# Kernel tuning notes

Hardware: AMD Instinct MI355X
Metric: run time of the kernel (lower is better)

Reference implementation:

```python
import jax, jax.numpy as jnp
import numpy as np

LN_EPS = 1e-5


def layer_norm(x, g, b):
    m = jnp.mean(x, axis=-1, keepdims=True)
    v = jnp.mean((x - m) ** 2, axis=-1, keepdims=True)
    return (x - m) * jax.lax.rsqrt(v + LN_EPS) * g + b


def setup_inputs() -> dict:
    key = jax.random.key(0)
    ks = jax.random.split(key, 8)
    B, S, D, C = 32, 512, 768, 25
    return {
        "bert_feature": jax.random.normal(ks[0], (B, S, D), dtype=jnp.float32),
        "output_encoder": jax.random.normal(ks[1], (B, S, D), dtype=jnp.float32),
        "cos_sim": jax.random.normal(ks[2], (B, S, C), dtype=jnp.float32),
        "decoder_embedding": jax.random.normal(ks[3], (B, C, D), dtype=jnp.float32),
        "labels": jax.random.randint(ks[4], (B, S), 0, C, dtype=jnp.int32),
        "ln_gamma": jnp.ones((D,), dtype=jnp.float32),
        "ln_beta": jnp.zeros((D,), dtype=jnp.float32),
        "W_add": jax.random.normal(ks[5], (D, C), dtype=jnp.float32) * 0.02,
        "b_add": jnp.zeros((C,), dtype=jnp.float32),
        "start_trans": jax.random.normal(ks[6], (C,), dtype=jnp.float32) * 0.1,
        "end_trans": jax.random.normal(ks[7], (C,), dtype=jnp.float32) * 0.1,
        "trans": jax.random.normal(jax.random.fold_in(key, 99), (C, C), dtype=jnp.float32) * 0.1,
    }


def crf_neg_log_likelihood(emissions, tags, start, end, trans):
    # emissions [B,S,C] (log-probs), tags [B,S]; no mask (all valid), torchcrf semantics
    B, S, C = emissions.shape
    b = jnp.arange(B)
    # numerator (gold path score)
    em_sc = jnp.take_along_axis(emissions, tags[:, :, None], axis=2)[..., 0].sum(axis=1)
    tr_sc = trans[tags[:, :-1], tags[:, 1:]].sum(axis=1)
    num = start[tags[:, 0]] + em_sc + tr_sc + end[tags[:, -1]]
    # partition function via forward algorithm (scan over time)
    def step(score, em_t):  # score [B,C]
        ns = jax.nn.logsumexp(score[:, :, None] + trans[None] + em_t[:, None, :], axis=1)
        return ns, None
    score0 = start[None] + emissions[:, 0]
    scoreT, _ = jax.lax.scan(step, score0, jnp.swapaxes(emissions[:, 1:], 0, 1))
    logZ = jax.nn.logsumexp(scoreT + end[None], axis=1)
    llh = num - logZ
    return llh.mean()  # reduction='mean'


def crf_decode(emissions, start, end, trans):
    # Viterbi; emissions [B,S,C]
    B, S, C = emissions.shape
    def vstep(score, em_t):
        cand = score[:, :, None] + trans[None]      # [B, prev, cur]
        best = jnp.max(cand, axis=1) + em_t
        idx = jnp.argmax(cand, axis=1)              # [B, cur] -> best prev tag
        return best, idx
    score0 = start[None] + emissions[:, 0]
    scoreT, hist = jax.lax.scan(vstep, score0, jnp.swapaxes(emissions[:, 1:], 0, 1))
    last = jnp.argmax(scoreT + end[None], axis=1)   # [B]
    def back(tag, h):
        prev = jnp.take_along_axis(h, tag[:, None], axis=1)[:, 0]
        return prev, prev
    _, prevs = jax.lax.scan(back, last, hist, reverse=True)
    return jnp.concatenate([prevs, last[None]], axis=0).T  # [B,S]


def reference(bert_feature, output_encoder, cos_sim, decoder_embedding, labels,
              ln_gamma, ln_beta, W_add, b_add, start_trans, end_trans, trans):
    # dropout is identity at eval time
    bf = layer_norm(bert_feature, ln_gamma, ln_beta)
    # prob_times_query: triple python loop == bmm(cos_sim, LN(decoder_embedding))
    # NOTE: original (faithfully) passes raw cos_sim, not its softmax.
    dec = layer_norm(decoder_embedding, ln_gamma, ln_beta)
    prob_query = jnp.einsum('bsc,bcd->bsd', cos_sim, dec)
    emb = layer_norm(bf + output_encoder + prob_query, ln_gamma, ln_beta)
    emb = jax.nn.relu(emb)
    ner_prob = jax.nn.log_softmax(emb @ W_add + b_add, axis=-1)  # [B,S,C]
    cos_sim_prob = jax.nn.softmax(cos_sim, axis=-1)
    llh = crf_neg_log_likelihood(ner_prob, labels, start_trans, end_trans, trans)
    loss = -llh  # model returns -1 * crf_loss
    path = crf_decode(cos_sim_prob, start_trans, end_trans, trans)
    return loss, path
```

## Files before the change

kernel.cpp:

```cpp
#include <hip/hip_runtime.h>
#include <hip/hip_bf16.h>


#define NEGINF (-1e30f)

__device__ __forceinline__ float rlane(float x, int i) {
  return __int_as_float(__builtin_amdgcn_readlane(__float_as_int(x), i));
}
__device__ __forceinline__ float rfl(float x) {
  return __int_as_float(__builtin_amdgcn_readfirstlane(__float_as_int(x)));
}
template <int CTRL, int RMASK>
__device__ __forceinline__ float dppAdd(float x) {
  return x + __int_as_float(__builtin_amdgcn_update_dpp(
                 0, __float_as_int(x), CTRL, RMASK, 0xF, true));
}
__device__ __forceinline__ float wsum(float v) {
  v = dppAdd<0x111, 0xF>(v);
  v = dppAdd<0x112, 0xF>(v);
  v = dppAdd<0x114, 0xF>(v);
  v = dppAdd<0x118, 0xF>(v);
  v = dppAdd<0x142, 0xA>(v);
  v = dppAdd<0x143, 0xC>(v);
  return rlane(v, 63);
}
__device__ __forceinline__ ushort f2bf(float x) {
  __hip_bfloat16 h = __float2bfloat16(x);
  return *reinterpret_cast<ushort*>(&h);
}
__device__ __forceinline__ void ld12(float* x, const float* p, int lane) {
#pragma unroll
  for (int k = 0; k < 3; k++) {
    float4 v = *(const float4*)(p + (lane + (k << 6)) * 4);
    x[4 * k + 0] = v.x; x[4 * k + 1] = v.y; x[4 * k + 2] = v.z; x[4 * k + 3] = v.w;
  }
}
__device__ __forceinline__ void ld12bf(float* x, const ushort* row, int lane) {
  uint2 d0 = *(const uint2*)((const char*)row + lane * 8);
  uint2 d1 = *(const uint2*)((const char*)row + lane * 8 + 512);
  uint2 d2 = *(const uint2*)((const char*)row + lane * 8 + 1024);
  x[0]  = __uint_as_float(d0.x << 16); x[1]  = __uint_as_float(d0.x & 0xffff0000u);
  x[2]  = __uint_as_float(d0.y << 16); x[3]  = __uint_as_float(d0.y & 0xffff0000u);
  x[4]  = __uint_as_float(d1.x << 16); x[5]  = __uint_as_float(d1.x & 0xffff0000u);
  x[6]  = __uint_as_float(d1.y << 16); x[7]  = __uint_as_float(d1.y & 0xffff0000u);
  x[8]  = __uint_as_float(d2.x << 16); x[9]  = __uint_as_float(d2.x & 0xffff0000u);
  x[10] = __uint_as_float(d2.y << 16); x[11] = __uint_as_float(d2.y & 0xffff0000u);
}

__device__ __forceinline__ float max25(const float c[25]) {
  float m0 = fmaxf(fmaxf(c[0], c[1]), c[2]);
  float m1 = fmaxf(fmaxf(c[3], c[4]), c[5]);
  float m2 = fmaxf(fmaxf(c[6], c[7]), c[8]);
  float m3 = fmaxf(fmaxf(c[9], c[10]), c[11]);
  float m4 = fmaxf(fmaxf(c[12], c[13]), c[14]);
  float m5 = fmaxf(fmaxf(c[15], c[16]), c[17]);
  float m6 = fmaxf(fmaxf(c[18], c[19]), c[20]);
  float m7 = fmaxf(fmaxf(c[21], c[22]), c[23]);
  float n0 = fmaxf(fmaxf(m0, m1), m2);
  float n1 = fmaxf(fmaxf(m3, m4), m5);
  float n2 = fmaxf(fmaxf(m6, m7), c[24]);
  return fmaxf(fmaxf(n0, n1), n2);
}

__device__ __forceinline__ void argmax25(const float c[25], float& bv, int& bi) {
  float v[13]; int x[13];
#pragma unroll
  for (int i = 0; i < 12; i++) {
    bool t = c[2 * i + 1] > c[2 * i];
    v[i] = t ? c[2 * i + 1] : c[2 * i];
    x[i] = t ? 2 * i + 1 : 2 * i;
  }
  v[12] = c[24]; x[12] = 24;
  float w[7]; int y[7];
#pragma unroll
  for (int i = 0; i < 6; i++) {
    bool t = v[2 * i + 1] > v[2 * i];
    w[i] = t ? v[2 * i + 1] : v[2 * i];
    y[i] = t ? x[2 * i + 1] : x[2 * i];
  }
  w[6] = v[12]; y[6] = x[12];
  float u[4]; int z[4];
#pragma unroll
  for (int i = 0; i < 3; i++) {
    bool t = w[2 * i + 1] > w[2 * i];
    u[i] = t ? w[2 * i + 1] : w[2 * i];
    z[i] = t ? y[2 * i + 1] : y[2 * i];
  }
  u[3] = w[6]; z[3] = y[6];
  bool t0 = u[1] > u[0]; float a = t0 ? u[1] : u[0]; int ai = t0 ? z[1] : z[0];
  bool t1 = u[3] > u[2]; float b = t1 ? u[3] : u[2]; int bj = t1 ? z[3] : z[2];
  bool t2 = b > a; bv = t2 ? b : a; bi = t2 ? bj : ai;
}

__global__ __launch_bounds__(256) void prep_kernel(
    const float* __restrict__ decemb, const float* __restrict__ gamma,
    const float* __restrict__ beta, const float* __restrict__ Wadd,
    const float* __restrict__ cosim,
    ushort* __restrict__ decb, ushort* __restrict__ wtb, float* __restrict__ csp) {
  const int blk = blockIdx.x;
  const int tid = threadIdx.x;
  __shared__ float sa[4], sq[4];
  __shared__ float sem[12800];
  if (blk < 800) {
    const float* in = decemb + (size_t)blk * 768;
    float x0 = in[tid], x1 = in[tid + 256], x2 = in[tid + 512];
    float s = x0 + x1 + x2, q = x0 * x0 + x1 * x1 + x2 * x2;
    float ws_ = wsum(s), wq = wsum(q);
    int w = tid >> 6, ln = tid & 63;
    if (ln == 0) { sa[w] = ws_; sq[w] = wq; }
    __syncthreads();
    float s1 = sa[0] + sa[1] + sa[2] + sa[3];
    float s2 = sq[0] + sq[1] + sq[2] + sq[3];
    float mean = s1 * (1.f / 768.f);
    float rstd = rsqrtf(s2 * (1.f / 768.f) - mean * mean + 1e-5f);
    ushort* o = decb + (size_t)blk * 768;
    o[tid]       = f2bf((x0 - mean) * rstd * gamma[tid]       + beta[tid]);
    o[tid + 256] = f2bf((x1 - mean) * rstd * gamma[tid + 256] + beta[tid + 256]);
    o[tid + 512] = f2bf((x2 - mean) * rstd * gamma[tid + 512] + beta[tid + 512]);
  } else if (blk < 832) {
    int gid = (blk - 800) * 256 + tid;
    for (int e = gid; e < 19200; e += 32 * 256) {
      int d = e / 25, j = e - d * 25;
      wtb[j * 768 + d] = f2bf(Wadd[e]);
    }
  } else {
    const int b = blk - 832;
    const float4* cb4 = (const float4*)(cosim + (size_t)b * 12800);
    float4* em4 = (float4*)sem;
    for (int i = tid; i < 3200; i += 256) em4[i] = cb4[i];
    __syncthreads();
#pragma unroll
    for (int rr = 0; rr < 2; rr++) {
      const int r = tid + (rr << 8);
      float v[25];
#pragma unroll
      for (int k = 0; k < 25; k++) v[k] = sem[r * 25 + k];
      float m01 = v[0];
#pragma unroll
      for (int k = 1; k < 25; k++) m01 = fmaxf(m01, v[k]);
      float s = 0.f;
#pragma unroll
      for (int k = 0; k < 25; k++) { v[k] = __expf(v[k] - m01); s += v[k]; }
      float rinv = __builtin_amdgcn_rcpf(s);
#pragma unroll
      for (int k = 0; k < 25; k++) sem[r * 25 + k] = v[k] * rinv;
    }
    __syncthreads();
    float4* cp4 = (float4*)(csp + (size_t)b * 12800);
    for (int i = tid; i < 3200; i += 256) cp4[i] = em4[i];
  }
}

__global__ __launch_bounds__(256) void main_kernel(
    const float* __restrict__ bert, const float* __restrict__ oenc,
    const float* __restrict__ cosim, const float* __restrict__ gamma,
    const float* __restrict__ beta, const float* __restrict__ badd,
    const ushort* __restrict__ decb, const ushort* __restrict__ wtb,
    const float* __restrict__ csp, const float* __restrict__ startt,
    const float* __restrict__ endt, const float* __restrict__ trans,
    float* __restrict__ nprob, float* __restrict__ traceF,
    float* __restrict__ traceB, float* __restrict__ out) {
  __shared__ ushort sh[19200];
  const int tid = threadIdx.x;
  const int lane = tid & 63;
  const int wid = tid >> 6;
  const int bid = blockIdx.x;

  if (bid < 64) {
    const bool isFwd = bid < 32;
    const int b = isFwd ? bid : bid - 32;
    const int tl = (lane < 25) ? lane : 24;
    float* em = (float*)sh;
    {
      const float4* src4 = (const float4*)(csp + (size_t)b * 12800 + (isFwd ? 0 : 6300));
      float4* dst4 = (float4*)em;
#pragma unroll
      for (int i = 0; i < 7; i++) {
        int e = tid + (i << 8);
        if (e < 1625) dst4[e] = src4[e];
      }
    }
    __syncthreads();
    if (wid != 0) return;

    __builtin_amdgcn_s_setprio(1);
    if (isFwd) {
      float* tf = traceF + (size_t)b * 16448;
      float Tc[25];
#pragma unroll
      for (int i = 0; i < 25; i++) Tc[i] = trans[i * 25 + tl];
      float sc = startt[tl] + em[tl];
      tf[lane] = sc;
      float emA = em[25 + tl], emB = em[50 + tl];
      for (int t = 1; t <= 256; t++) {
        float emC = em[(t + 2) * 25 + tl];
        float s[25], c[25];
#pragma unroll
        for (int i = 0; i < 25; i++) s[i] = rlane(sc, i);
#pragma unroll
        for (int i = 0; i < 25; i++) c[i] = s[i] + Tc[i];
        float bv = max25(c);
        sc = bv + emA;
        tf[t * 64 + lane] = sc;
        emA = emB; emB = emC;
      }
    } else {
      float* tb = traceB + (size_t)b * 16448;
      float Tr[25];
#pragma unroll
      for (int j = 0; j < 25; j++) Tr[j] = trans[tl * 25 + j];
      float bwd = endt[tl];
      float emA = em[(511 - 252) * 25 + tl], emB = em[(510 - 252) * 25 + tl];
      for (int t = 511; t >= 257; t--) {
        float emC = em[(t - 2 - 252) * 25 + tl];
        tb[(511 - t) * 64 + lane] = bwd;
        float u = bwd + emA;
        float s[25], c[25];
#pragma unroll
        for (int j = 0; j < 25; j++) s[j] = rlane(u, j);
#pragma unroll
        for (int j = 0; j < 25; j++) c[j] = s[j] + Tr[j];
        float bv = max25(c);
        bwd = bv;
        emA = emB; emB = emC;
      }
      tb[255 * 64 + lane] = bwd;
    }
    __builtin_amdgcn_s_setprio(0);
    return;
  }

  if (bid == 64 && tid == 0) out[0] = 0.f;
  const int idx = bid - 64;
  const int swz = (idx & 7) * 256 + (idx >> 3);
  const int b = swz >> 6;
  const int rowg = b * 512 + ((swz & 63) << 3) + (wid << 1);

  {
    const uint4* src = (const uint4*)(decb + (size_t)b * 19200);
    uint4* dst = (uint4*)sh;
#pragma unroll
    for (int i = 0; i < 10; i++) {
      int e = tid + (i << 8);
      if (e < 2400) dst[e] = src[e];
    }
  }
  float g[12], bbv[12];
  ld12(g, gamma, lane);
  ld12(bbv, beta, lane);
  float acc[2][12];
  ld12(acc[0], bert + (size_t)(rowg + 0) * 768, lane);
  ld12(acc[1], bert + (size_t)(rowg + 1) * 768, lane);
  float cs0 = (lane < 25) ? cosim[(size_t)(rowg + 0) * 25 + lane] : 0.f;
  float cs1 = (lane < 25) ? cosim[(size_t)(rowg + 1) * 25 + lane] : 0.f;
  __syncthreads();

#pragma unroll
  for (int r = 0; r < 2; r++) {
    float s = 0.f, q = 0.f;
#pragma unroll
    for (int e = 0; e < 12; e++) { s += acc[r][e]; q += acc[r][e] * acc[r][e]; }
    s = wsum(s); q = wsum(q);
    float mean = s * (1.f / 768.f);
    float rstd = rsqrtf(q * (1.f / 768.f) - mean * mean + 1e-5f);
#pragma unroll
    for (int e = 0; e < 12; e++) acc[r][e] = (acc[r][e] - mean) * rstd * g[e] + bbv[e];
  }

  const char* sd = (const char*)sh;
#pragma unroll 5
  for (int c = 0; c < 25; c++) {
    uint2 d0 = *(const uint2*)(sd + c * 1536 + lane * 8);
    uint2 d1 = *(const uint2*)(sd + c * 1536 + lane * 8 + 512);
    uint2 d2 = *(const uint2*)(sd + c * 1536 + lane * 8 + 1024);
    float dv[12];
    dv[0]  = __uint_as_float(d0.x << 16); dv[1]  = __uint_as_float(d0.x & 0xffff0000u);
    dv[2]  = __uint_as_float(d0.y << 16); dv[3]  = __uint_as_float(d0.y & 0xffff0000u);
    dv[4]  = __uint_as_float(d1.x << 16); dv[5]  = __uint_as_float(d1.x & 0xffff0000u);
    dv[6]  = __uint_as_float(d1.y << 16); dv[7]  = __uint_as_float(d1.y & 0xffff0000u);
    dv[8]  = __uint_as_float(d2.x << 16); dv[9]  = __uint_as_float(d2.x & 0xffff0000u);
    dv[10] = __uint_as_float(d2.y << 16); dv[11] = __uint_as_float(d2.y & 0xffff0000u);
    float f0 = rlane(cs0, c), f1 = rlane(cs1, c);
#pragma unroll
    for (int e = 0; e < 12; e++) {
      acc[0][e] = fmaf(f0, dv[e], acc[0][e]);
      acc[1][e] = fmaf(f1, dv[e], acc[1][e]);
    }
  }

#pragma unroll
  for (int r = 0; r < 2; r++) {
    float y[12];
    ld12(y, oenc + (size_t)(rowg + r) * 768, lane);
#pragma unroll
    for (int e = 0; e < 12; e++) acc[r][e] += y[e];
  }

#pragma unroll
  for (int r = 0; r < 2; r++) {
    float s = 0.f, q = 0.f;
#pragma unroll
    for (int e = 0; e < 12; e++) { s += acc[r][e]; q += acc[r][e] * acc[r][e]; }
    s = wsum(s); q = wsum(q);
    float mean = s * (1.f / 768.f);
    float rstd = rsqrtf(q * (1.f / 768.f) - mean * mean + 1e-5f);
#pragma unroll
    for (int e = 0; e < 12; e++)
      acc[r][e] = fmaxf((acc[r][e] - mean) * rstd * g[e] + bbv[e], 0.f);
  }

  __syncthreads();

  ushort* scw0 = sh + wid * 3400;
  ushort* scw1 = scw0 + 1700;
#pragma unroll 5
  for (int j = 0; j < 25; j++) {
    float wv[12];
    ld12bf(wv, wtb + j * 768, lane);
    float p0 = 0.f, p1 = 0.f;
#pragma unroll
    for (int e = 0; e < 12; e++) {
      p0 = fmaf(acc[0][e], wv[e], p0);
      p1 = fmaf(acc[1][e], wv[e], p1);
    }
    scw0[j * 68 + lane] = f2bf(p0);
    scw1[j * 68 + lane] = f2bf(p1);
  }
  float bav = (lane < 25) ? badd[lane] : 0.f;
  const int jj = (lane < 25) ? lane : 24;
#pragma unroll
  for (int r = 0; r < 2; r++) {
    const ushort* scw = (r == 0) ? scw0 : scw1;
    float lg = bav;
#pragma unroll
    for (int i = 0; i < 16; i++) {
      uint2 u = *(const uint2*)(scw + jj * 68 + i * 4);
      lg += __uint_as_float(u.x << 16);
      lg += __uint_as_float(u.x & 0xffff0000u);
      lg += __uint_as_float(u.y << 16);
      lg += __uint_as_float(u.y & 0xffff0000u);
    }
    float v = (lane < 25) ? lg : NEGINF;
    float m = rfl(lg);
    float e = __expf(v - m);
    float s = wsum(e);
    if (lane < 25) nprob[(size_t)(rowg + r) * 25 + lane] = e * __builtin_amdgcn_rcpf(s);
  }
}

__global__ __launch_bounds__(256) void scan_kernel(
    const float* __restrict__ nprob, const float* __restrict__ csp,
    const float* __restrict__ traceF, const float* __restrict__ traceB,
    const int* __restrict__ labels, const float* __restrict__ startt,
    const float* __restrict__ endt, const float* __restrict__ trans,
    float* __restrict__ out) {
  const int tid = threadIdx.x, lane = tid & 63, wid = tid >> 6;
  const int blk = blockIdx.x;
  const int tl = (lane < 25) ? lane : 24;
  __shared__ __align__(16) unsigned char shraw[13568];

  if (blk < 32) {
    const int b = blk;
    const float* np = nprob + (size_t)b * 12800;
    float* fp = (float*)shraw;
    float* fq = fp + 32;
    float* snum = fq + 32;
    int* sKf = (int*)(snum + 1);
    int* sKb = sKf + 1;
    if (wid == 0) {
      float Mc[25];
#pragma unroll
      for (int i = 0; i < 25; i++) Mc[i] = __expf(trans[i * 25 + tl]);
      float p = (lane < 25) ? __expf(startt[lane]) * np[lane] : 0.f;
      float eA = np[25 + tl], eB = np[50 + tl];
      int K = 0;
      for (int t = 1; t <= 256; t++) {
        float eC = np[(t + 2) * 25 + tl];
        float s[25];
#pragma unroll
        for (int i = 0; i < 25; i++) s[i] = rlane(p, i);
        float a0 = 0, a1 = 0, a2 = 0, a3 = 0, a4 = 0;
#pragma unroll
        for (int i = 0; i < 25; i += 5) {
          a0 = fmaf(s[i + 0], Mc[i + 0], a0);
          a1 = fmaf(s[i + 1], Mc[i + 1], a1);
          a2 = fmaf(s[i + 2], Mc[i + 2], a2);
          a3 = fmaf(s[i + 3], Mc[i + 3], a3);
          a4 = fmaf(s[i + 4], Mc[i + 4], a4);
        }
        float acc = ((a0 + a1) + (a2 + a3)) + a4;
        if ((t & 7) == 0) {
          unsigned mu = 0;
#pragma unroll
          for (int i = 0; i < 25; i++) {
            unsigned ub = __float_as_uint(s[i]);
            mu = (ub > mu) ? ub : mu;
          }
          int e8 = (int)((mu >> 23) & 0xFF);
          acc *= __uint_as_float((unsigned)(254 - e8) << 23);
          K += 127 - e8;
        }
        p = (lane < 25) ? acc * eA : 0.f;
        eA = eB; eB = eC;
      }
      if (lane < 25) fp[lane] = p;
      if (lane == 0) *sKf = K;
    } else if (wid == 1) {
      float MrE[25];
#pragma unroll
      for (int j = 0; j < 25; j++) MrE[j] = __expf(trans[tl * 25 + j]);
      float q = (lane < 25) ? __expf(endt[lane]) : 0.f;
      float eA = np[511 * 25 + tl], eB = np[510 * 25 + tl];
      int K = 0;
      for (int t = 511; t >= 257; t--) {
        float eC = np[(t - 2) * 25 + tl];
        float u = q * eA;
        float s[25];
#pragma unroll
        for (int j = 0; j < 25; j++) s[j] = rlane(u, j);
        float a0 = 0, a1 = 0, a2 = 0, a3 = 0, a4 = 0;
#pragma unroll
        for (int j = 0; j < 25; j += 5) {
          a0 = fmaf(s[j + 0], MrE[j + 0], a0);
          a1 = fmaf(s[j + 1], MrE[j + 1], a1);
          a2 = fmaf(s[j + 2], MrE[j + 2], a2);
          a3 = fmaf(s[j + 3], MrE[j + 3], a3);
          a4 = fmaf(s[j + 4], MrE[j + 4], a4);
        }
        float acc = ((a0 + a1) + (a2 + a3)) + a4;
        if ((t & 7) == 0) {
          unsigned mu = 0;
#pragma unroll
          for (int j = 0; j < 25; j++) {
            unsigned ub = __float_as_uint(s[j]);
            mu = (ub > mu) ? ub : mu;
          }
          int e8 = (int)((mu >> 23) & 0xFF);
          acc *= __uint_as_float((unsigned)(254 - e8) << 23);
          K += 127 - e8;
        }
        q = (lane < 25) ? acc : 0.f;
        eA = eB; eB = eC;
      }
      if (lane < 25) fq[lane] = q;
      if (lane == 0) *sKb = K;
    } else if (wid == 2) {
      float a = 0.f;
      const int* lb = labels + b * 512;
      for (int t = lane; t < 512; t += 64) a += __logf(np[t * 25 + lb[t]]);
      for (int t = lane; t < 511; t += 64) a += trans[lb[t] * 25 + lb[t + 1]];
      a = wsum(a);
      if (lane == 0) *snum = a + startt[lb[0]] + endt[lb[511]];
    }
    __syncthreads();
    if (wid == 0) {
      float z = (lane < 25) ? fp[lane] * fq[lane] : 0.f;
      z = wsum(z);
      float logZ = __logf(z) - (float)(*sKf + *sKb) * 0.6931471805599453f;
      float llh = *snum - logZ;
      if (lane == 0) atomicAdd(out, -llh * (1.f / 32.f));
    }
    return;
  }

  const int vb = blk - 32;
  const int b = vb & 31;
  const bool isFwd = vb < 32;
  unsigned char* hist = shraw;
  const float* tf = traceF + (size_t)b * 16448;
  const float* tb = traceB + (size_t)b * 16448;

  if (isFwd) {
    float Tc[25];
#pragma unroll
    for (int i = 0; i < 25; i++) Tc[i] = trans[i * 25 + tl];
    int t0 = 1 + (wid << 6);
    float vA = tf[(t0 - 1) * 64 + tl];
    for (int n = 0; n < 64; n++) {
      int t = t0 + n;
      float vB = (n < 63) ? tf[t * 64 + tl] : 0.f;
      float s[25], c[25];
#pragma unroll
      for (int i = 0; i < 25; i++) s[i] = rlane(vA, i);
#pragma unroll
      for (int i = 0; i < 25; i++) c[i] = s[i] + Tc[i];
      float bv; int bi;
      argmax25(c, bv, bi);
      if (lane < 25) hist[t * 26 + lane] = (unsigned char)bi;
      vA = vB;
    }
  } else {
    float Tr[25];
#pragma unroll
    for (int j = 0; j < 25; j++) Tr[j] = trans[tl * 25 + j];
    const float* cb = csp + (size_t)b * 12800;
    int t0 = 257 + (wid << 6);
    float tA = (t0 <= 511) ? tb[(511 - t0) * 64 + tl] : 0.f;
    float eA = (t0 <= 511) ? cb[t0 * 25 + tl] : 0.f;
    for (int n = 0; n < 64; n++) {
      int t = t0 + n;
      if (t > 511) break;
      float tBn = (t < 511) ? tb[(511 - t - 1) * 64 + tl] : 0.f;
      float eBn = (t < 511) ? cb[(t + 1) * 25 + tl] : 0.f;
      float u = tA + eA;
      float s[25], c[25];
#pragma unroll
      for (int j = 0; j < 25; j++) s[j] = rlane(u, j);
#pragma unroll
      for (int j = 0; j < 25; j++) c[j] = s[j] + Tr[j];
      float bv; int bj;
      argmax25(c, bv, bj);
      if (lane < 25) hist[t * 26 + lane] = (unsigned char)bj;
      tA = tBn; eA = eBn;
    }
  }
  __syncthreads();
  if (wid == 0) {
    float fv = (lane < 25) ? tf[256 * 64 + lane] + tb[255 * 64 + lane] : NEGINF;
    int idx = lane;
#pragma unroll
    for (int m = 32; m >= 1; m >>= 1) {
      float ov = __shfl_xor(fv, m); int oi = __shfl_xor(idx, m);
      if (ov > fv || (ov == fv && oi < idx)) { fv = ov; idx = oi; }
    }
    int cur = idx;
    float* path = out + 1 + (size_t)b * 512;
    if (isFwd) {
      if (lane == 0) path[256] = (float)cur;
      int h = (lane < 25) ? hist[256 * 26 + lane] : 0;
      for (int t = 256; t >= 1; t--) {
        int hn = (t > 1 && lane < 25) ? hist[(t - 1) * 26 + lane] : 0;
        int prev = __builtin_amdgcn_readlane(h, cur);
        if (lane == 0) path[t - 1] = (float)prev;
        cur = prev; h = hn;
      }
    } else {
      int h = (lane < 25) ? hist[257 * 26 + lane] : 0;
      for (int t = 257; t <= 511; t++) {
        int hn = (t < 511 && lane < 25) ? hist[(t + 1) * 26 + lane] : 0;
        int nx = __builtin_amdgcn_readlane(h, cur);
        if (lane == 0) path[t] = (float)nx;
        cur = nx; h = hn;
      }
    }
  }
}

extern "C" void kernel_launch(void* const* d_in, const int* in_sizes, int n_in,
                              void* d_out, int out_size, void* d_ws, size_t ws_size,
                              hipStream_t stream) {
  (void)in_sizes; (void)n_in; (void)out_size; (void)ws_size;
  const float* bert   = (const float*)d_in[0];
  const float* oenc   = (const float*)d_in[1];
  const float* cosim  = (const float*)d_in[2];
  const float* decemb = (const float*)d_in[3];
  const int*   labels = (const int*)d_in[4];
  const float* gamma  = (const float*)d_in[5];
  const float* beta   = (const float*)d_in[6];
  const float* Wadd   = (const float*)d_in[7];
  const float* badd   = (const float*)d_in[8];
  const float* startt = (const float*)d_in[9];
  const float* endt   = (const float*)d_in[10];
  const float* trans  = (const float*)d_in[11];
  float* out = (float*)d_out;
  char*  wsb = (char*)d_ws;
  ushort* decb   = (ushort*)wsb;
  ushort* wtb    = (ushort*)(wsb + 1228800);
  float*  nprob  = (float*)(wsb + 1305600);
  float*  csp    = (float*)(wsb + 2944000);
  float*  traceF = (float*)(wsb + 4582400);
  float*  traceB = (float*)(wsb + 6687744);

  prep_kernel<<<864, 256, 0, stream>>>(decemb, gamma, beta, Wadd, cosim, decb, wtb, csp);
  main_kernel<<<2112, 256, 0, stream>>>(bert, oenc, cosim, gamma, beta, badd, decb, wtb,
                                        csp, startt, endt, trans, nprob, traceF, traceB, out);
  scan_kernel<<<96, 256, 0, stream>>>(nprob, csp, traceF, traceB, labels, startt, endt,
                                      trans, out);
}
```

Before: 105.1 us.

## Use 512-thread main blocks and compute logits from LDS-staged W with wave reductions

The main kernel now runs 512-thread blocks covering 16 rows each instead of 256-thread blocks covering 8, and the grid shrinks to match. The projection onto the 25 classes is restructured. The bf16 weight matrix is first copied into shared memory, reusing the space that held the decoder embedding. Each logit is then formed by a full-wave DPP reduction per class instead of storing bf16 partial sums to LDS and re-summing them transposed. This removes the partial-sum scratch and its bf16 rounding, but adds 50 serialized wave reductions per wave and an extra block-wide barrier.

```diff
diff --git a/kernel.cpp b/kernel.cpp
--- a/kernel.cpp
+++ b/kernel.cpp
@@ -151,7 +151,7 @@
   }
 }
 
-__global__ __launch_bounds__(256) void main_kernel(
+__global__ __launch_bounds__(512) void main_kernel(
     const float* __restrict__ bert, const float* __restrict__ oenc,
     const float* __restrict__ cosim, const float* __restrict__ gamma,
     const float* __restrict__ beta, const float* __restrict__ badd,
@@ -175,8 +175,8 @@
       const float4* src4 = (const float4*)(csp + (size_t)b * 12800 + (isFwd ? 0 : 6300));
       float4* dst4 = (float4*)em;
 #pragma unroll
-      for (int i = 0; i < 7; i++) {
-        int e = tid + (i << 8);
+      for (int i = 0; i < 4; i++) {
+        int e = tid + (i << 9);
         if (e < 1625) dst4[e] = src4[e];
       }
     }
@@ -232,16 +232,16 @@
 
   if (bid == 64 && tid == 0) out[0] = 0.f;
   const int idx = bid - 64;
-  const int swz = (idx & 7) * 256 + (idx >> 3);
-  const int b = swz >> 6;
-  const int rowg = b * 512 + ((swz & 63) << 3) + (wid << 1);
+  const int swz = (idx & 7) * 128 + (idx >> 3);
+  const int b = swz >> 5;
+  const int rowg = b * 512 + ((swz & 31) << 4) + (wid << 1);
 
   {
     const uint4* src = (const uint4*)(decb + (size_t)b * 19200);
     uint4* dst = (uint4*)sh;
 #pragma unroll
-    for (int i = 0; i < 10; i++) {
-      int e = tid + (i << 8);
+    for (int i = 0; i < 5; i++) {
+      int e = tid + (i << 9);
       if (e < 2400) dst[e] = src[e];
     }
   }
@@ -310,38 +310,33 @@
   }
 
   __syncthreads();
-
-  ushort* scw0 = sh + wid * 3400;
-  ushort* scw1 = scw0 + 1700;
-#pragma unroll 5
-  for (int j = 0; j < 25; j++) {
-    float wv[12];
-    ld12bf(wv, wtb + j * 768, lane);
-    float p0 = 0.f, p1 = 0.f;
-#pragma unroll
-    for (int e = 0; e < 12; e++) {
-      p0 = fmaf(acc[0][e], wv[e], p0);
-      p1 = fmaf(acc[1][e], wv[e], p1);
-    }
-    scw0[j * 68 + lane] = f2bf(p0);
-    scw1[j * 68 + lane] = f2bf(p1);
-  }
+  {
+    const uint4* src = (const uint4*)wtb;
+    uint4* dst = (uint4*)sh;
+#pragma unroll
+    for (int i = 0; i < 5; i++) {
+      int e = tid + (i << 9);
+      if (e < 2400) dst[e] = src[e];
+    }
+  }
+  __syncthreads();
+
   float bav = (lane < 25) ? badd[lane] : 0.f;
-  const int jj = (lane < 25) ? lane : 24;
 #pragma unroll
   for (int r = 0; r < 2; r++) {
-    const ushort* scw = (r == 0) ? scw0 : scw1;
-    float lg = bav;
-#pragma unroll
-    for (int i = 0; i < 16; i++) {
-      uint2 u = *(const uint2*)(scw + jj * 68 + i * 4);
-      lg += __uint_as_float(u.x << 16);
-      lg += __uint_as_float(u.x & 0xffff0000u);
-      lg += __uint_as_float(u.y << 16);
-      lg += __uint_as_float(u.y & 0xffff0000u);
-    }
-    float v = (lane < 25) ? lg : NEGINF;
-    float m = rfl(lg);
+    float lg = 0.f;
+#pragma unroll
+    for (int j = 0; j < 25; j++) {
+      float wv[12];
+      ld12bf(wv, sh + j * 768, lane);
+      float p = 0.f;
+#pragma unroll
+      for (int e = 0; e < 12; e++) p = fmaf(acc[r][e], wv[e], p);
+      float sj = wsum(p);
+      lg = (lane == j) ? sj : lg;
+    }
+    float v = (lane < 25) ? (lg + bav) : NEGINF;
+    float m = rfl(v);
     float e = __expf(v - m);
     float s = wsum(e);
     if (lane < 25) nprob[(size_t)(rowg + r) * 25 + lane] = e * __builtin_amdgcn_rcpf(s);
@@ -572,7 +567,7 @@
   float*  traceB = (float*)(wsb + 6687744);
 
   prep_kernel<<<864, 256, 0, stream>>>(decemb, gamma, beta, Wadd, cosim, decb, wtb, csp);
-  main_kernel<<<2112, 256, 0, stream>>>(bert, oenc, cosim, gamma, beta, badd, decb, wtb,
+  main_kernel<<<1088, 512, 0, stream>>>(bert, oenc, cosim, gamma, beta, badd, decb, wtb,
                                         csp, startt, endt, trans, nprob, traceF, traceB, out);
   scan_kernel<<<96, 256, 0, stream>>>(nprob, csp, traceF, traceB, labels, startt, endt,
                                       trans, out);
```

Measured after the change: 111.5 us. 1.06x slower.
